# Kernel tuning notes

Hardware: AMD Instinct MI355X
Metric: run time of the kernel (lower is better)

The kernel has to match this reference:

```python
import jax, jax.numpy as jnp
import numpy as np

N = 50000      # nodes
E = 800000     # edges (before self-loops)
DIN = 384
D = 128        # hidden_dim == output_dim
H = 4          # heads
FH = D // H    # per-head dim
B = 64         # graphs in batch
NEG = 0.2      # LeakyReLU slope in GATConv
EPS = 1e-5     # LayerNorm eps


def setup_inputs() -> dict:
    key = jax.random.key(0)
    ks = jax.random.split(key, 24)
    s = 0.02
    inp = {
        'node_features': jax.random.normal(ks[0], (N, DIN), jnp.float32),
        'edge_index': jax.random.randint(ks[1], (2, E), 0, N, dtype=jnp.int64),
        'edge_weight': jax.random.uniform(ks[2], (E,), jnp.float32),
        'batch': jnp.sort(jax.random.randint(ks[3], (N,), 0, B, dtype=jnp.int64)),
        # input projection
        'Wp': jax.random.normal(ks[4], (DIN, D), jnp.float32) * s,
        'bp': jnp.zeros((D,), jnp.float32),
    }
    for l in range(2):
        o = 5 + l * 9
        inp[f'W{l}'] = jax.random.normal(ks[o], (D, D), jnp.float32) * s      # lin_src (shared src/dst)
        inp[f'as{l}'] = jax.random.normal(ks[o + 1], (H, FH), jnp.float32) * s  # att_src
        inp[f'ad{l}'] = jax.random.normal(ks[o + 2], (H, FH), jnp.float32) * s  # att_dst
        inp[f'We{l}'] = jax.random.normal(ks[o + 3], (D,), jnp.float32) * s   # lin_edge (edge_dim=1)
        inp[f'ae{l}'] = jax.random.normal(ks[o + 4], (H, FH), jnp.float32) * s  # att_edge
        inp[f'b{l}'] = jnp.zeros((D,), jnp.float32)                           # GATConv bias
        inp[f'g{l}'] = jnp.ones((D,), jnp.float32)                            # LayerNorm gamma
        inp[f'be{l}'] = jnp.zeros((D,), jnp.float32)                          # LayerNorm beta
    return inp


def _gat(x, src, dst, ew, W, a_s, a_d, We, a_e, b):
    """PyG GATConv(in, D/H, heads=H, edge_dim=1), eval mode. ew includes self-loops."""
    n = x.shape[0]
    h = (x @ W).reshape(n, H, FH)                      # [N,H,FH]
    a_src = jnp.einsum('nhf,hf->nh', h, a_s)           # [N,H]
    a_dst = jnp.einsum('nhf,hf->nh', h, a_d)
    e = (ew[:, None] * We[None, :]).reshape(-1, H, FH)  # edge_dim=1 linear, no bias
    a_eg = jnp.einsum('ehf,hf->eh', e, a_e)            # [E,H]
    alpha = jax.nn.leaky_relu(a_src[src] + a_dst[dst] + a_eg, NEG)
    # softmax over incoming edges of each dst node
    amax = jax.ops.segment_max(alpha, dst, num_segments=n)
    amax = jnp.where(jnp.isfinite(amax), amax, 0.0)
    ex = jnp.exp(alpha - amax[dst])
    denom = jax.ops.segment_sum(ex, dst, num_segments=n)
    coef = ex / (denom[dst] + 1e-16)                   # [E,H]
    msg = h[src] * coef[..., None]                     # [E,H,FH]
    out = jax.ops.segment_sum(msg, dst, num_segments=n).reshape(n, D)
    return out + b


def _ln(x, g, b):
    mu = x.mean(-1, keepdims=True)
    v = ((x - mu) ** 2).mean(-1, keepdims=True)
    return (x - mu) * jax.lax.rsqrt(v + EPS) * g + b


def reference(node_features, edge_index, edge_weight, batch, Wp, bp,
              W0, as0, ad0, We0, ae0, b0, g0, be0,
              W1, as1, ad1, We1, ae1, b1, g1, be1):
    n = node_features.shape[0]
    # PyG GATConv add_self_loops=True, fill_value='mean' for edge_attr
    loop = jnp.arange(n, dtype=edge_index.dtype)
    src = jnp.concatenate([edge_index[0], loop])
    dst = jnp.concatenate([edge_index[1], loop])
    ew = jnp.concatenate([edge_weight, jnp.full((n,), edge_weight.mean(), edge_weight.dtype)])

    x = node_features @ Wp + bp
    for (W, a_s, a_d, We, a_e, b, g, be) in (
        (W0, as0, ad0, We0, ae0, b0, g0, be0),
        (W1, as1, ad1, We1, ae1, b1, g1, be1),
    ):
        res = x
        y = _gat(x, src, dst, ew, W, a_s, a_d, We, a_e, b)
        y = jax.nn.elu(_ln(y, g, be))
        x = y + res  # shapes match (hidden == output)

    # global_mean_pool
    s = jax.ops.segment_sum(x, batch, num_segments=B)
    c = jax.ops.segment_sum(jnp.ones((n,), x.dtype), batch, num_segments=B)
    return s / jnp.maximum(c, 1.0)[:, None]
```

## Files before the change

kernel.cpp:

```cpp
#include <hip/hip_runtime.h>

#define N_NODES 50000
#define N_EDGES 800000
#define DIN 384
#define DH 128
#define NB 64
#define NEG 0.2f

__device__ __forceinline__ float bf2f(unsigned short u) {
    return __uint_as_float((unsigned)u << 16);
}
__device__ __forceinline__ unsigned short f2bf(float x) {
    unsigned u = __float_as_uint(x);
    return (unsigned short)((u + 0x7fff + ((u >> 16) & 1)) >> 16);
}
__device__ __forceinline__ float sel4(float4 v, int k) {
    float r = v.x;
    r = (k == 1) ? v.y : r;
    r = (k == 2) ? v.z : r;
    r = (k == 3) ? v.w : r;
    return r;
}
using us8 = __attribute__((ext_vector_type(8))) unsigned short;

__global__ __launch_bounds__(256) void histew_kernel(const int* __restrict__ dst,
                                                     const float* __restrict__ ew,
                                                     int* __restrict__ cnt,
                                                     int* __restrict__ rank,
                                                     float* __restrict__ ews) {
    __shared__ float sred[4];
    const int tid = threadIdx.x;
    float v = 0.0f;
    for (int i = blockIdx.x * 256 + tid; i < N_EDGES; i += gridDim.x * 256) {
        rank[i] = atomicAdd(&cnt[dst[i]], 1);
        v += ew[i];
    }
    #pragma unroll
    for (int o = 32; o; o >>= 1) v += __shfl_down(v, o, 64);
    if ((tid & 63) == 0) sred[tid >> 6] = v;
    __syncthreads();
    if (tid == 0) atomicAdd(ews, sred[0] + sred[1] + sred[2] + sred[3]);
}

__global__ void scan_a(const int* __restrict__ cnt, int* __restrict__ scanned,
                       int* __restrict__ bsums) {
    __shared__ int s[256];
    int tid = threadIdx.x;
    int i = blockIdx.x * 256 + tid;
    int v = (i < N_NODES) ? cnt[i] : 0;
    s[tid] = v; __syncthreads();
    for (int o = 1; o < 256; o <<= 1) {
        int t = (tid >= o) ? s[tid - o] : 0;
        __syncthreads();
        s[tid] += t;
        __syncthreads();
    }
    if (i < N_NODES) scanned[i] = s[tid] - v;
    if (tid == 255) bsums[blockIdx.x] = s[255];
}

__global__ void scan_b(int* __restrict__ bsums, int nb,
                       const float* __restrict__ We0, const float* __restrict__ ae0,
                       const float* __restrict__ We1, const float* __restrict__ ae1,
                       const float* __restrict__ ews, float* __restrict__ consts) {
    __shared__ int s[256];
    int tid = threadIdx.x;
    int v = (tid < nb) ? bsums[tid] : 0;
    s[tid] = v; __syncthreads();
    for (int o = 1; o < 256; o <<= 1) {
        int t = (tid >= o) ? s[tid - o] : 0;
        __syncthreads();
        s[tid] += t;
        __syncthreads();
    }
    if (tid < nb) bsums[tid] = s[tid] - v;

    if (tid < 64) {
        const int l = tid;
        float p00 = We0[l] * ae0[l];
        float p01 = We0[l + 64] * ae0[l + 64];
        float p10 = We1[l] * ae1[l];
        float p11 = We1[l + 64] * ae1[l + 64];
        #pragma unroll
        for (int o = 1; o < 32; o <<= 1) {
            p00 += __shfl_xor(p00, o, 64); p01 += __shfl_xor(p01, o, 64);
            p10 += __shfl_xor(p10, o, 64); p11 += __shfl_xor(p11, o, 64);
        }
        const float c0 = __shfl(p00, 0, 64), c1 = __shfl(p00, 32, 64);
        const float c2 = __shfl(p01, 0, 64), c3 = __shfl(p01, 32, 64);
        const float d0 = __shfl(p10, 0, 64), d1 = __shfl(p10, 32, 64);
        const float d2 = __shfl(p11, 0, 64), d3 = __shfl(p11, 32, 64);
        if (l == 0) {
            consts[0] = c0; consts[1] = c1; consts[2] = c2; consts[3] = c3;
            consts[4] = d0; consts[5] = d1; consts[6] = d2; consts[7] = d3;
            consts[8] = ews[0] * (1.0f / N_EDGES);
        }
    }
}

__global__ void scan_c(const int* __restrict__ scanned, const int* __restrict__ bsums,
                       const int* __restrict__ cnt, int* __restrict__ ptr) {
    int i = blockIdx.x * 256 + threadIdx.x;
    if (i < N_NODES) {
        int p = scanned[i] + bsums[blockIdx.x];
        ptr[i] = p;
        if (i == N_NODES - 1) ptr[N_NODES] = p + cnt[i];
    }
}

__global__ __launch_bounds__(256) void fill_kernel(const int* __restrict__ src,
                            const int* __restrict__ dst,
                            const float* __restrict__ ew,
                            const int* __restrict__ rank,
                            const int* __restrict__ ptr,
                            int2* __restrict__ recE) {
    const int e0 = (blockIdx.x * 256 + threadIdx.x) * 4;
    if (e0 >= N_EDGES) return;
    const int4 d4 = *(const int4*)(dst + e0);
    const int4 s4 = *(const int4*)(src + e0);
    const int4 r4 = *(const int4*)(rank + e0);
    const float4 w4 = *(const float4*)(ew + e0);
    recE[ptr[d4.x] + r4.x] = make_int2(s4.x, __float_as_int(w4.x));
    recE[ptr[d4.y] + r4.y] = make_int2(s4.y, __float_as_int(w4.y));
    recE[ptr[d4.z] + r4.z] = make_int2(s4.z, __float_as_int(w4.z));
    recE[ptr[d4.w] + r4.w] = make_int2(s4.w, __float_as_int(w4.w));
}

template<int K, bool BF16OUT>
__global__ __launch_bounds__(256) void mfma_gemm(const float* __restrict__ A,
                                                 const float* __restrict__ W,
                                                 const float* __restrict__ bias,
                                                 void* __restrict__ Cv, int M,
                                                 const float* __restrict__ a_s,
                                                 const float* __restrict__ a_d,
                                                 float* __restrict__ asrc_o,
                                                 float* __restrict__ adst_o)
{
    constexpr int BM = 64, BK = 32;
    constexpr int LS = 40;
    __shared__ unsigned short As[BM * LS];
    __shared__ unsigned short Bs[DH * LS];
    using short8 = __attribute__((ext_vector_type(8))) short;
    using f32x4  = __attribute__((ext_vector_type(4))) float;

    const int tid = threadIdx.x;
    const int w = tid >> 6, l = tid & 63;
    const int lane16 = l & 15, quad = l >> 4;
    const int m0 = blockIdx.x * BM;

    f32x4 acc[8] = {};

    const int ar = tid >> 2, af = tid & 3;
    int arow = m0 + ar; if (arow >= M) arow = M - 1;
    const float* Ap = A + (size_t)arow * K;
    const int bn = tid & 127, bq = tid >> 7;

    for (int k0 = 0; k0 < K; k0 += BK) {
        __syncthreads();
        #pragma unroll
        for (int i = 0; i < 2; ++i) {
            const int f4 = af + 4 * i;
            float4 v = *(const float4*)(Ap + k0 + f4 * 4);
            ushort4 u = {f2bf(v.x), f2bf(v.y), f2bf(v.z), f2bf(v.w)};
            *(ushort4*)&As[ar * LS + f4 * 4] = u;
        }
        #pragma unroll
        for (int i = 0; i < 4; ++i) {
            const int kq = bq + 2 * i;
            float v0 = W[(size_t)(k0 + kq * 4 + 0) * DH + bn];
            float v1 = W[(size_t)(k0 + kq * 4 + 1) * DH + bn];
            float v2 = W[(size_t)(k0 + kq * 4 + 2) * DH + bn];
            float v3 = W[(size_t)(k0 + kq * 4 + 3) * DH + bn];
            ushort4 u = {f2bf(v0), f2bf(v1), f2bf(v2), f2bf(v3)};
            *(ushort4*)&Bs[bn * LS + kq * 4] = u;
        }
        __syncthreads();
        short8 afrag = *(short8*)&As[(w * 16 + lane16) * LS + quad * 8];
        #pragma unroll
        for (int nt = 0; nt < 8; ++nt) {
            short8 bfrag = *(short8*)&Bs[(nt * 16 + lane16) * LS + quad * 8];
            acc[nt] = __builtin_amdgcn_mfma_f32_16x16x32_bf16(afrag, bfrag, acc[nt], 0, 0, 0);
        }
    }

    const int orow0 = m0 + w * 16 + quad * 4;
    #pragma unroll
    for (int nt = 0; nt < 8; ++nt) {
        const int col = nt * 16 + lane16;
        const float bv = BF16OUT ? 0.0f : bias[col];
        #pragma unroll
        for (int r = 0; r < 4; ++r) {
            const int row = orow0 + r;
            if (row < M) {
                if constexpr (BF16OUT)
                    ((unsigned short*)Cv)[(size_t)row * DH + col] = f2bf(acc[nt][r]);
                else
                    ((float*)Cv)[(size_t)row * DH + col] = acc[nt][r] + bv;
            }
        }
    }

    if constexpr (BF16OUT) {
        float psh[4][4] = {}, pdh[4][4] = {};
        #pragma unroll
        for (int nt = 0; nt < 8; ++nt) {
            const int hd = nt >> 1;
            const float asv = a_s[nt * 16 + lane16];
            const float adv = a_d[nt * 16 + lane16];
            #pragma unroll
            for (int r = 0; r < 4; ++r) {
                psh[hd][r] = fmaf(acc[nt][r], asv, psh[hd][r]);
                pdh[hd][r] = fmaf(acc[nt][r], adv, pdh[hd][r]);
            }
        }
        #pragma unroll
        for (int o = 1; o < 16; o <<= 1) {
            #pragma unroll
            for (int hd = 0; hd < 4; ++hd)
                #pragma unroll
                for (int r = 0; r < 4; ++r) {
                    psh[hd][r] += __shfl_xor(psh[hd][r], o, 64);
                    pdh[hd][r] += __shfl_xor(pdh[hd][r], o, 64);
                }
        }
        if (lane16 == 0) {
            #pragma unroll
            for (int r = 0; r < 4; ++r) {
                const int row = orow0 + r;
                if (row < M) {
                    float4 o1 = {psh[0][r], psh[1][r], psh[2][r], psh[3][r]};
                    float4 o2 = {pdh[0][r], pdh[1][r], pdh[2][r], pdh[3][r]};
                    *(float4*)(asrc_o + (size_t)row * 4) = o1;
                    *(float4*)(adst_o + (size_t)row * 4) = o2;
                }
            }
        }
    }
}

#define MSG_NPB 4
#define MSG_GRID 2048
__global__ __launch_bounds__(256) void msg_kernel(
    const unsigned short* __restrict__ h, const float* __restrict__ asrc,
    const float* __restrict__ adst, const float* __restrict__ xres,
    const int* __restrict__ indptr, const int2* __restrict__ recE,
    const float* __restrict__ consts, const int layer,
    const float* __restrict__ bias, const float* __restrict__ gamma,
    const float* __restrict__ beta, float* __restrict__ xout)
{
    const int l = threadIdx.x & 63;
    const int wv = threadIdx.x >> 6;
    const int sub2 = l >> 4, c8 = l & 15, hd8 = c8 >> 2;

    const float4 ccv = *(const float4*)(consts + layer * 4);
    const float cc_l = sel4(ccv, hd8);
    const float ewm = consts[8];
    const unsigned short* hb = h + c8 * 8;

    for (int n = blockIdx.x * MSG_NPB + wv; n < N_NODES; n += MSG_GRID * MSG_NPB) {
        const int st = indptr[n];
        const int deg = indptr[n + 1] - st;
        const float4 ad4 = *(const float4*)(adst + (size_t)n * 4);
        const float4 as4 = *(const float4*)(asrc + (size_t)n * 4);
        const float ad_l = sel4(ad4, hd8);
        const float as_l = sel4(as4, hd8);
        float a0 = as_l + ad_l + ewm * cc_l;
        a0 = a0 > 0.f ? a0 : NEG * a0;
        const float pv0_l = __expf(a0);

        float dsum = 0.f;
        float acc8[8] = {};
        if (sub2 == 0) {
            us8 u = *(const us8*)(hb + (size_t)n * DH);
            #pragma unroll
            for (int i = 0; i < 8; ++i) acc8[i] = pv0_l * bf2f(u[i]);
        }

        const int2* rq = recE + st;
        int e = sub2;
        for (; e + 12 < deg; e += 16) {
            const int2 r0 = rq[e],     r1 = rq[e + 4];
            const int2 r2 = rq[e + 8], r3 = rq[e + 12];
            const float av0 = asrc[(size_t)r0.x * 4 + hd8];
            const float av1 = asrc[(size_t)r1.x * 4 + hd8];
            const float av2 = asrc[(size_t)r2.x * 4 + hd8];
            const float av3 = asrc[(size_t)r3.x * 4 + hd8];
            us8 u0 = *(const us8*)(hb + (size_t)r0.x * DH);
            us8 u1 = *(const us8*)(hb + (size_t)r1.x * DH);
            us8 u2 = *(const us8*)(hb + (size_t)r2.x * DH);
            us8 u3 = *(const us8*)(hb + (size_t)r3.x * DH);
            float al0 = av0 + ad_l + __int_as_float(r0.y) * cc_l;
            float al1 = av1 + ad_l + __int_as_float(r1.y) * cc_l;
            float al2 = av2 + ad_l + __int_as_float(r2.y) * cc_l;
            float al3 = av3 + ad_l + __int_as_float(r3.y) * cc_l;
            al0 = al0 > 0.f ? al0 : NEG * al0;
            al1 = al1 > 0.f ? al1 : NEG * al1;
            al2 = al2 > 0.f ? al2 : NEG * al2;
            al3 = al3 > 0.f ? al3 : NEG * al3;
            const float c0 = __expf(al0), c1 = __expf(al1);
            const float c2 = __expf(al2), c3 = __expf(al3);
            dsum += (c0 + c1) + (c2 + c3);
            #pragma unroll
            for (int i = 0; i < 8; ++i)
                acc8[i] = fmaf(c0, bf2f(u0[i]),
                          fmaf(c1, bf2f(u1[i]),
                          fmaf(c2, bf2f(u2[i]),
                          fmaf(c3, bf2f(u3[i]), acc8[i]))));
        }
        for (; e < deg; e += 4) {
            const int2 r = rq[e];
            const float av = asrc[(size_t)r.x * 4 + hd8];
            us8 u = *(const us8*)(hb + (size_t)r.x * DH);
            float al = av + ad_l + __int_as_float(r.y) * cc_l;
            al = al > 0.f ? al : NEG * al;
            const float c = __expf(al);
            dsum += c;
            #pragma unroll
            for (int i = 0; i < 8; ++i) acc8[i] = fmaf(c, bf2f(u[i]), acc8[i]);
        }

        #pragma unroll
        for (int i = 0; i < 8; ++i) {
            acc8[i] += __shfl_xor(acc8[i], 16, 64);
            acc8[i] += __shfl_xor(acc8[i], 32, 64);
        }
        dsum += __shfl_xor(dsum, 16, 64);
        dsum += __shfl_xor(dsum, 32, 64);

        const float inv_d = 1.0f / (dsum + pv0_l + 1e-16f);
        const float4 b4a = *(const float4*)(bias + c8 * 8);
        const float4 b4b = *(const float4*)(bias + c8 * 8 + 4);
        float y[8];
        y[0] = acc8[0] * inv_d + b4a.x; y[1] = acc8[1] * inv_d + b4a.y;
        y[2] = acc8[2] * inv_d + b4a.z; y[3] = acc8[3] * inv_d + b4a.w;
        y[4] = acc8[4] * inv_d + b4b.x; y[5] = acc8[5] * inv_d + b4b.y;
        y[6] = acc8[6] * inv_d + b4b.z; y[7] = acc8[7] * inv_d + b4b.w;

        float s1 = 0.f, s2 = 0.f;
        #pragma unroll
        for (int i = 0; i < 8; ++i) { s1 += y[i]; s2 += y[i] * y[i]; }
        #pragma unroll
        for (int o = 1; o < 16; o <<= 1) {
            s1 += __shfl_xor(s1, o, 64);
            s2 += __shfl_xor(s2, o, 64);
        }
        const float mu = s1 * (1.0f / DH);
        const float var = s2 * (1.0f / DH) - mu * mu;
        const float rs = rsqrtf(var + 1e-5f);

        if (sub2 == 0) {
            const float4 g4a = *(const float4*)(gamma + c8 * 8);
            const float4 g4b = *(const float4*)(gamma + c8 * 8 + 4);
            const float4 e4a = *(const float4*)(beta + c8 * 8);
            const float4 e4b = *(const float4*)(beta + c8 * 8 + 4);
            const float4 r4a = *(const float4*)(xres + (size_t)n * DH + c8 * 8);
            const float4 r4b = *(const float4*)(xres + (size_t)n * DH + c8 * 8 + 4);
            const float gv[8] = {g4a.x, g4a.y, g4a.z, g4a.w, g4b.x, g4b.y, g4b.z, g4b.w};
            const float ev[8] = {e4a.x, e4a.y, e4a.z, e4a.w, e4b.x, e4b.y, e4b.z, e4b.w};
            const float rv[8] = {r4a.x, r4a.y, r4a.z, r4a.w, r4b.x, r4b.y, r4b.z, r4b.w};
            float z[8];
            #pragma unroll
            for (int i = 0; i < 8; ++i) {
                float t = (y[i] - mu) * rs * gv[i] + ev[i];
                z[i] = (t > 0.f ? t : __expf(t) - 1.0f) + rv[i];
            }
            *(float4*)(xout + (size_t)n * DH + c8 * 8)     = *(float4*)&z[0];
            *(float4*)(xout + (size_t)n * DH + c8 * 8 + 4) = *(float4*)&z[4];
        }
    }
}

#define PNODES 64
__global__ __launch_bounds__(128) void pool_kernel(const float* __restrict__ x,
        const int* __restrict__ batch, float* __restrict__ pool, int* __restrict__ gcnt)
{
    int t = threadIdx.x;
    int n0 = blockIdx.x * PNODES;
    if (n0 >= N_NODES) return;
    int n1 = min(n0 + PNODES, N_NODES);
    float acc = 0.f; int cn = 0;
    int curb = batch[n0];
    for (int n = n0; n < n1; ++n) {
        int b = batch[n];
        if (b != curb) {
            atomicAdd(&pool[(size_t)curb * DH + t], acc);
            if (t == 0) atomicAdd(&gcnt[curb], cn);
            acc = 0.f; cn = 0; curb = b;
        }
        acc += x[(size_t)n * DH + t];
        ++cn;
    }
    atomicAdd(&pool[(size_t)curb * DH + t], acc);
    if (t == 0) atomicAdd(&gcnt[curb], cn);
}

__global__ void div_kernel(const float* __restrict__ pool, const int* __restrict__ gcnt,
                           float* __restrict__ out)
{
    int i = blockIdx.x * blockDim.x + threadIdx.x;
    if (i < NB * DH) {
        float c = (float)gcnt[i >> 7];
        out[i] = pool[i] / fmaxf(c, 1.0f);
    }
}

extern "C" void kernel_launch(void* const* d_in, const int* in_sizes, int n_in,
                              void* d_out, int out_size, void* d_ws, size_t ws_size,
                              hipStream_t stream)
{
    const float* nf    = (const float*)d_in[0];
    const int*   esrc  = (const int*)d_in[1];
    const int*   edst  = esrc + N_EDGES;
    const float* ew    = (const float*)d_in[2];
    const int*   batch = (const int*)d_in[3];
    const float* Wp    = (const float*)d_in[4];
    const float* bp    = (const float*)d_in[5];
    const float* Wl[2]  = {(const float*)d_in[6],  (const float*)d_in[14]};
    const float* asl[2] = {(const float*)d_in[7],  (const float*)d_in[15]};
    const float* adl[2] = {(const float*)d_in[8],  (const float*)d_in[16]};
    const float* Wel[2] = {(const float*)d_in[9],  (const float*)d_in[17]};
    const float* ael[2] = {(const float*)d_in[10], (const float*)d_in[18]};
    const float* bl[2]  = {(const float*)d_in[11], (const float*)d_in[19]};
    const float* gl[2]  = {(const float*)d_in[12], (const float*)d_in[20]};
    const float* bel[2] = {(const float*)d_in[13], (const float*)d_in[21]};
    float* outp = (float*)d_out;

    char* w = (char*)d_ws;
    auto alloc = [&](size_t bytes) { char* p = w; w += (bytes + 255) & ~255ull; return p; };
    float* xA     = (float*)alloc((size_t)N_NODES * DH * 4);
    float* xB     = (float*)alloc((size_t)N_NODES * DH * 4);
    unsigned short* hbuf = (unsigned short*)alloc((size_t)N_NODES * DH * 2);
    float* asrc   = (float*)alloc((size_t)N_NODES * 4 * 4);
    float* adst   = (float*)alloc((size_t)N_NODES * 4 * 4);
    float* pool   = (float*)alloc((size_t)NB * DH * 4);
    int* gcnt     = (int*)alloc(256);
    float* ews    = (float*)alloc(256);
    int* cnt      = (int*)alloc((size_t)N_NODES * 4);
    int* scanned  = (int*)alloc((size_t)N_NODES * 4);
    int* bsums    = (int*)alloc(1024);
    int* ptr      = (int*)alloc((size_t)(N_NODES + 8) * 4);
    int* rank     = (int*)alloc((size_t)N_EDGES * 4);
    int2* recE    = (int2*)alloc((size_t)N_EDGES * 8);
    float* consts = (float*)alloc(256);

    hipMemsetAsync(pool, 0, (size_t)NB * DH * 4 + 256 + 256 + (size_t)N_NODES * 4, stream);

    const int sb = (N_NODES + 255) / 256;

    histew_kernel<<<1024, 256, 0, stream>>>(edst, ew, cnt, rank, ews);
    scan_a<<<sb, 256, 0, stream>>>(cnt, scanned, bsums);
    scan_b<<<1, 256, 0, stream>>>(bsums, sb, Wel[0], ael[0], Wel[1], ael[1], ews, consts);
    scan_c<<<sb, 256, 0, stream>>>(scanned, bsums, cnt, ptr);
    fill_kernel<<<(N_EDGES / 4 + 255) / 256, 256, 0, stream>>>(esrc, edst, ew, rank, ptr, recE);

    const int gb = (N_NODES + 63) / 64;
    mfma_gemm<DIN, false><<<gb, 256, 0, stream>>>(nf, Wp, bp, xA, N_NODES,
                                                  nullptr, nullptr, nullptr, nullptr);

    const float* xin = xA;
    float* xout = xB;
    for (int l = 0; l < 2; ++l) {
        mfma_gemm<DH, true><<<gb, 256, 0, stream>>>(xin, Wl[l], nullptr, hbuf, N_NODES,
                                                    asl[l], adl[l], asrc, adst);
        msg_kernel<<<MSG_GRID, 256, 0, stream>>>(
            hbuf, asrc, adst, xin, ptr, recE, consts, l,
            bl[l], gl[l], bel[l], xout);
        float* tmp = (float*)xin; xin = xout; xout = tmp;
    }

    pool_kernel<<<(N_NODES + PNODES - 1) / PNODES, 128, 0, stream>>>(xin, batch, pool, gcnt);
    div_kernel<<<(NB * DH + 255) / 256, 256, 0, stream>>>(pool, gcnt, outp);
}
```

Before: 418.5 us.

## Map one 16-lane group per node in GAT message kernel, drop grid-stride loop

The message-passing kernel previously gave each wave one node and split that node's edges across four 16-lane sub-groups, then combined them with cross-lane shuffles. Now each 16-lane group owns a whole node and walks all its edges serially. The persistent grid-stride loop is replaced by one launch covering every node. This removes the cross-subgroup reductions and the masked residual work, and puts four nodes in flight per wave. In exchange there is more per-lane serial latency for high-degree nodes, possible load imbalance inside a wave, and no bounds check, so it relies on N_NODES being divisible by 16.

```diff
diff --git a/kernel.cpp b/kernel.cpp
--- a/kernel.cpp
+++ b/kernel.cpp
@@ -238,8 +238,7 @@
     }
 }
 
-#define MSG_NPB 4
-#define MSG_GRID 2048
+#define MSG_NPB 16
 __global__ __launch_bounds__(256) void msg_kernel(
     const unsigned short* __restrict__ h, const float* __restrict__ asrc,
     const float* __restrict__ adst, const float* __restrict__ xres,
@@ -250,124 +249,115 @@
 {
     const int l = threadIdx.x & 63;
     const int wv = threadIdx.x >> 6;
-    const int sub2 = l >> 4, c8 = l & 15, hd8 = c8 >> 2;
+    const int grp = l >> 4;
+    const int c8 = l & 15;
+    const int hd8 = c8 >> 2;
+
+    const int n = blockIdx.x * MSG_NPB + wv * 4 + grp;
 
     const float4 ccv = *(const float4*)(consts + layer * 4);
     const float cc_l = sel4(ccv, hd8);
     const float ewm = consts[8];
     const unsigned short* hb = h + c8 * 8;
 
-    for (int n = blockIdx.x * MSG_NPB + wv; n < N_NODES; n += MSG_GRID * MSG_NPB) {
-        const int st = indptr[n];
-        const int deg = indptr[n + 1] - st;
-        const float4 ad4 = *(const float4*)(adst + (size_t)n * 4);
-        const float4 as4 = *(const float4*)(asrc + (size_t)n * 4);
-        const float ad_l = sel4(ad4, hd8);
-        const float as_l = sel4(as4, hd8);
-        float a0 = as_l + ad_l + ewm * cc_l;
-        a0 = a0 > 0.f ? a0 : NEG * a0;
-        const float pv0_l = __expf(a0);
-
-        float dsum = 0.f;
-        float acc8[8] = {};
-        if (sub2 == 0) {
-            us8 u = *(const us8*)(hb + (size_t)n * DH);
-            #pragma unroll
-            for (int i = 0; i < 8; ++i) acc8[i] = pv0_l * bf2f(u[i]);
-        }
-
-        const int2* rq = recE + st;
-        int e = sub2;
-        for (; e + 12 < deg; e += 16) {
-            const int2 r0 = rq[e],     r1 = rq[e + 4];
-            const int2 r2 = rq[e + 8], r3 = rq[e + 12];
-            const float av0 = asrc[(size_t)r0.x * 4 + hd8];
-            const float av1 = asrc[(size_t)r1.x * 4 + hd8];
-            const float av2 = asrc[(size_t)r2.x * 4 + hd8];
-            const float av3 = asrc[(size_t)r3.x * 4 + hd8];
-            us8 u0 = *(const us8*)(hb + (size_t)r0.x * DH);
-            us8 u1 = *(const us8*)(hb + (size_t)r1.x * DH);
-            us8 u2 = *(const us8*)(hb + (size_t)r2.x * DH);
-            us8 u3 = *(const us8*)(hb + (size_t)r3.x * DH);
-            float al0 = av0 + ad_l + __int_as_float(r0.y) * cc_l;
-            float al1 = av1 + ad_l + __int_as_float(r1.y) * cc_l;
-            float al2 = av2 + ad_l + __int_as_float(r2.y) * cc_l;
-            float al3 = av3 + ad_l + __int_as_float(r3.y) * cc_l;
-            al0 = al0 > 0.f ? al0 : NEG * al0;
-            al1 = al1 > 0.f ? al1 : NEG * al1;
-            al2 = al2 > 0.f ? al2 : NEG * al2;
-            al3 = al3 > 0.f ? al3 : NEG * al3;
-            const float c0 = __expf(al0), c1 = __expf(al1);
-            const float c2 = __expf(al2), c3 = __expf(al3);
-            dsum += (c0 + c1) + (c2 + c3);
-            #pragma unroll
-            for (int i = 0; i < 8; ++i)
-                acc8[i] = fmaf(c0, bf2f(u0[i]),
-                          fmaf(c1, bf2f(u1[i]),
-                          fmaf(c2, bf2f(u2[i]),
-                          fmaf(c3, bf2f(u3[i]), acc8[i]))));
-        }
-        for (; e < deg; e += 4) {
-            const int2 r = rq[e];
-            const float av = asrc[(size_t)r.x * 4 + hd8];
-            us8 u = *(const us8*)(hb + (size_t)r.x * DH);
-            float al = av + ad_l + __int_as_float(r.y) * cc_l;
-            al = al > 0.f ? al : NEG * al;
-            const float c = __expf(al);
-            dsum += c;
-            #pragma unroll
-            for (int i = 0; i < 8; ++i) acc8[i] = fmaf(c, bf2f(u[i]), acc8[i]);
-        }
-
-        #pragma unroll
-        for (int i = 0; i < 8; ++i) {
-            acc8[i] += __shfl_xor(acc8[i], 16, 64);
-            acc8[i] += __shfl_xor(acc8[i], 32, 64);
-        }
-        dsum += __shfl_xor(dsum, 16, 64);
-        dsum += __shfl_xor(dsum, 32, 64);
-
-        const float inv_d = 1.0f / (dsum + pv0_l + 1e-16f);
-        const float4 b4a = *(const float4*)(bias + c8 * 8);
-        const float4 b4b = *(const float4*)(bias + c8 * 8 + 4);
-        float y[8];
-        y[0] = acc8[0] * inv_d + b4a.x; y[1] = acc8[1] * inv_d + b4a.y;
-        y[2] = acc8[2] * inv_d + b4a.z; y[3] = acc8[3] * inv_d + b4a.w;
-        y[4] = acc8[4] * inv_d + b4b.x; y[5] = acc8[5] * inv_d + b4b.y;
-        y[6] = acc8[6] * inv_d + b4b.z; y[7] = acc8[7] * inv_d + b4b.w;
-
-        float s1 = 0.f, s2 = 0.f;
-        #pragma unroll
-        for (int i = 0; i < 8; ++i) { s1 += y[i]; s2 += y[i] * y[i]; }
-        #pragma unroll
-        for (int o = 1; o < 16; o <<= 1) {
-            s1 += __shfl_xor(s1, o, 64);
-            s2 += __shfl_xor(s2, o, 64);
-        }
-        const float mu = s1 * (1.0f / DH);
-        const float var = s2 * (1.0f / DH) - mu * mu;
-        const float rs = rsqrtf(var + 1e-5f);
-
-        if (sub2 == 0) {
-            const float4 g4a = *(const float4*)(gamma + c8 * 8);
-            const float4 g4b = *(const float4*)(gamma + c8 * 8 + 4);
-            const float4 e4a = *(const float4*)(beta + c8 * 8);
-            const float4 e4b = *(const float4*)(beta + c8 * 8 + 4);
-            const float4 r4a = *(const float4*)(xres + (size_t)n * DH + c8 * 8);
-            const float4 r4b = *(const float4*)(xres + (size_t)n * DH + c8 * 8 + 4);
-            const float gv[8] = {g4a.x, g4a.y, g4a.z, g4a.w, g4b.x, g4b.y, g4b.z, g4b.w};
-            const float ev[8] = {e4a.x, e4a.y, e4a.z, e4a.w, e4b.x, e4b.y, e4b.z, e4b.w};
-            const float rv[8] = {r4a.x, r4a.y, r4a.z, r4a.w, r4b.x, r4b.y, r4b.z, r4b.w};
-            float z[8];
-            #pragma unroll
-            for (int i = 0; i < 8; ++i) {
-                float t = (y[i] - mu) * rs * gv[i] + ev[i];
-                z[i] = (t > 0.f ? t : __expf(t) - 1.0f) + rv[i];
-            }
-            *(float4*)(xout + (size_t)n * DH + c8 * 8)     = *(float4*)&z[0];
-            *(float4*)(xout + (size_t)n * DH + c8 * 8 + 4) = *(float4*)&z[4];
-        }
-    }
+    const int st = indptr[n];
+    const int deg = indptr[n + 1] - st;
+    const float ad_l = adst[(size_t)n * 4 + hd8];
+    const float as_l = asrc[(size_t)n * 4 + hd8];
+
+    float a0 = as_l + ad_l + ewm * cc_l;
+    a0 = a0 > 0.f ? a0 : NEG * a0;
+    const float pv0_l = __expf(a0);
+
+    float dsum = 0.f;
+    float acc8[8];
+    {
+        us8 u = *(const us8*)(hb + (size_t)n * DH);
+        #pragma unroll
+        for (int i = 0; i < 8; ++i) acc8[i] = pv0_l * bf2f(u[i]);
+    }
+
+    const int2* rq = recE + st;
+    int e = 0;
+    for (; e + 3 < deg; e += 4) {
+        const int2 r0 = rq[e],     r1 = rq[e + 1];
+        const int2 r2 = rq[e + 2], r3 = rq[e + 3];
+        const float av0 = asrc[(size_t)r0.x * 4 + hd8];
+        const float av1 = asrc[(size_t)r1.x * 4 + hd8];
+        const float av2 = asrc[(size_t)r2.x * 4 + hd8];
+        const float av3 = asrc[(size_t)r3.x * 4 + hd8];
+        us8 u0 = *(const us8*)(hb + (size_t)r0.x * DH);
+        us8 u1 = *(const us8*)(hb + (size_t)r1.x * DH);
+        us8 u2 = *(const us8*)(hb + (size_t)r2.x * DH);
+        us8 u3 = *(const us8*)(hb + (size_t)r3.x * DH);
+        float al0 = av0 + ad_l + __int_as_float(r0.y) * cc_l;
+        float al1 = av1 + ad_l + __int_as_float(r1.y) * cc_l;
+        float al2 = av2 + ad_l + __int_as_float(r2.y) * cc_l;
+        float al3 = av3 + ad_l + __int_as_float(r3.y) * cc_l;
+        al0 = al0 > 0.f ? al0 : NEG * al0;
+        al1 = al1 > 0.f ? al1 : NEG * al1;
+        al2 = al2 > 0.f ? al2 : NEG * al2;
+        al3 = al3 > 0.f ? al3 : NEG * al3;
+        const float c0 = __expf(al0), c1 = __expf(al1);
+        const float c2 = __expf(al2), c3 = __expf(al3);
+        dsum += (c0 + c1) + (c2 + c3);
+        #pragma unroll
+        for (int i = 0; i < 8; ++i)
+            acc8[i] = fmaf(c0, bf2f(u0[i]),
+                      fmaf(c1, bf2f(u1[i]),
+                      fmaf(c2, bf2f(u2[i]),
+                      fmaf(c3, bf2f(u3[i]), acc8[i]))));
+    }
+    for (; e < deg; ++e) {
+        const int2 r = rq[e];
+        const float av = asrc[(size_t)r.x * 4 + hd8];
+        us8 u = *(const us8*)(hb + (size_t)r.x * DH);
+        float al = av + ad_l + __int_as_float(r.y) * cc_l;
+        al = al > 0.f ? al : NEG * al;
+        const float c = __expf(al);
+        dsum += c;
+        #pragma unroll
+        for (int i = 0; i < 8; ++i) acc8[i] = fmaf(c, bf2f(u[i]), acc8[i]);
+    }
+
+    const float inv_d = 1.0f / (dsum + pv0_l + 1e-16f);
+    const float4 b4a = *(const float4*)(bias + c8 * 8);
+    const float4 b4b = *(const float4*)(bias + c8 * 8 + 4);
+    float y[8];
+    y[0] = acc8[0] * inv_d + b4a.x; y[1] = acc8[1] * inv_d + b4a.y;
+    y[2] = acc8[2] * inv_d + b4a.z; y[3] = acc8[3] * inv_d + b4a.w;
+    y[4] = acc8[4] * inv_d + b4b.x; y[5] = acc8[5] * inv_d + b4b.y;
+    y[6] = acc8[6] * inv_d + b4b.z; y[7] = acc8[7] * inv_d + b4b.w;
+
+    float s1 = 0.f, s2 = 0.f;
+    #pragma unroll
+    for (int i = 0; i < 8; ++i) { s1 += y[i]; s2 += y[i] * y[i]; }
+    #pragma unroll
+    for (int o = 1; o < 16; o <<= 1) {
+        s1 += __shfl_xor(s1, o, 64);
+        s2 += __shfl_xor(s2, o, 64);
+    }
+    const float mu = s1 * (1.0f / DH);
+    const float var = s2 * (1.0f / DH) - mu * mu;
+    const float rs = rsqrtf(var + 1e-5f);
+
+    const float4 g4a = *(const float4*)(gamma + c8 * 8);
+    const float4 g4b = *(const float4*)(gamma + c8 * 8 + 4);
+    const float4 e4a = *(const float4*)(beta + c8 * 8);
+    const float4 e4b = *(const float4*)(beta + c8 * 8 + 4);
+    const float4 r4a = *(const float4*)(xres + (size_t)n * DH + c8 * 8);
+    const float4 r4b = *(const float4*)(xres + (size_t)n * DH + c8 * 8 + 4);
+    const float gv[8] = {g4a.x, g4a.y, g4a.z, g4a.w, g4b.x, g4b.y, g4b.z, g4b.w};
+    const float ev[8] = {e4a.x, e4a.y, e4a.z, e4a.w, e4b.x, e4b.y, e4b.z, e4b.w};
+    const float rv[8] = {r4a.x, r4a.y, r4a.z, r4a.w, r4b.x, r4b.y, r4b.z, r4b.w};
+    float z[8];
+    #pragma unroll
+    for (int i = 0; i < 8; ++i) {
+        float t = (y[i] - mu) * rs * gv[i] + ev[i];
+        z[i] = (t > 0.f ? t : __expf(t) - 1.0f) + rv[i];
+    }
+    *(float4*)(xout + (size_t)n * DH + c8 * 8)     = *(float4*)&z[0];
+    *(float4*)(xout + (size_t)n * DH + c8 * 8 + 4) = *(float4*)&z[4];
 }
 
 #define PNODES 64
@@ -462,7 +452,7 @@
     for (int l = 0; l < 2; ++l) {
         mfma_gemm<DH, true><<<gb, 256, 0, stream>>>(xin, Wl[l], nullptr, hbuf, N_NODES,
                                                     asl[l], adl[l], asrc, adst);
-        msg_kernel<<<MSG_GRID, 256, 0, stream>>>(
+        msg_kernel<<<N_NODES / MSG_NPB, 256, 0, stream>>>(
             hbuf, asrc, adst, xin, ptr, recE, consts, l,
             bl[l], gl[l], bel[l], xout);
         float* tmp = (float*)xin; xin = xout; xout = tmp;
```

Result: faster. 378.4 us (-9.6%).
